# Performance work log

Measured on AMD Instinct MI355X. Metric: run time of the kernel, lower is better.

## Reference

```python
import jax, jax.numpy as jnp
import numpy as np

BIG_NUMBER = 1000000.0
B, N, H = 8, 256, 128   # batch, nodes, node/hidden feat
E, G = 128, 128         # edge feat, graph feat
MID, OUT = 128, 128
IN_Z = 2 * H


def setup_inputs() -> dict:
    key = jax.random.key(0)
    ks = jax.random.split(key, 20)
    sc = lambda fan_in: 1.0 / np.sqrt(fan_in)
    inp = {
        "node_fts": jax.random.normal(ks[0], (B, N, H), jnp.float32),
        "edge_fts": jax.random.normal(ks[1], (B, N, N, E), jnp.float32),
        "graph_fts": jax.random.normal(ks[2], (B, G), jnp.float32),
        "adj_mat": (jax.random.uniform(ks[3], (B, N, N)) < 0.5).astype(jnp.float32),
        "hidden": jax.random.normal(ks[4], (B, N, H), jnp.float32),
        # linear params, stored [in, out]
        "W1": jax.random.normal(ks[5], (IN_Z, MID), jnp.float32) * sc(IN_Z),
        "b1": jnp.zeros((MID,), jnp.float32),
        "W2": jax.random.normal(ks[6], (IN_Z, MID), jnp.float32) * sc(IN_Z),
        "b2": jnp.zeros((MID,), jnp.float32),
        "We": jax.random.normal(ks[7], (E, MID), jnp.float32) * sc(E),
        "be": jnp.zeros((MID,), jnp.float32),
        "Wg": jax.random.normal(ks[8], (G, MID), jnp.float32) * sc(G),
        "bg": jnp.zeros((MID,), jnp.float32),
        "Wo1": jax.random.normal(ks[9], (IN_Z, OUT), jnp.float32) * sc(IN_Z),
        "bo1": jnp.zeros((OUT,), jnp.float32),
        "Wo2": jax.random.normal(ks[10], (MID, OUT), jnp.float32) * sc(MID),
        "bo2": jnp.zeros((OUT,), jnp.float32),
    }
    return inp


def reference(node_fts, edge_fts, graph_fts, adj_mat, hidden,
              W1, b1, W2, b2, We, be, Wg, bg, Wo1, bo1, Wo2, bo2):
    # z: [b, n, 2h]
    z = jnp.concatenate([node_fts, hidden], axis=-1)
    msg_1 = z @ W1 + b1                       # [b, n, mid]
    msg_2 = z @ W2 + b2                       # [b, n, mid]
    msg_e = edge_fts @ We + be                # [b, n, n, mid]
    msg_g = graph_fts @ Wg + bg               # [b, mid]
    # msgs[b, i, j, :]; reduce over i (senders)
    msgs = (msg_1[:, None, :, :] + msg_2[:, :, None, :]
            + msg_e + msg_g[:, None, None, :])
    maxarg = jnp.where(adj_mat[..., None] > 0, msgs, -BIG_NUMBER)
    msgs_red = jnp.max(maxarg, axis=1)        # [b, n, mid]
    ret = jax.nn.relu((z @ Wo1 + bo1) + (msgs_red @ Wo2 + bo2))
    return ret
```

## Files before the change

kernel.cpp:

```cpp
#include <hip/hip_runtime.h>
#include <hip/hip_bf16.h>
#include <stdint.h>
#include <stddef.h>

#define B_   8
#define N_   256
#define H_   128
#define E_   128
#define INZ  256
#define BIGN 1000000.0f

typedef float f32x4 __attribute__((ext_vector_type(4)));
typedef short bf16x8 __attribute__((ext_vector_type(8)));

static __device__ __forceinline__ unsigned cvt2(float a, float b) {
    unsigned short ra = __builtin_bit_cast(unsigned short, __float2bfloat16(a));
    unsigned short rb = __builtin_bit_cast(unsigned short, __float2bfloat16(b));
    return (unsigned)ra | ((unsigned)rb << 16);
}

__global__ __launch_bounds__(256) void prep_kernel(
    const float* __restrict__ node, const float* __restrict__ hidden,
    const float* __restrict__ gf,
    const float* __restrict__ W1, const float* __restrict__ b1,
    const float* __restrict__ W2, const float* __restrict__ b2,
    const float* __restrict__ Wg, const float* __restrict__ bg,
    const float* __restrict__ Wo1, const float* __restrict__ bo1,
    const float* __restrict__ We,
    float* __restrict__ msg1, float* __restrict__ m2g,
    float* __restrict__ zo1, unsigned short* __restrict__ weT)
{
    __shared__ float zs[4][INZ];
    const int t  = threadIdx.x;
    const int r0 = blockIdx.x * 4;
    const int b  = r0 >> 8;

    for (int idx = t; idx < 4 * INZ; idx += 256) {
        int r = idx >> 8, k = idx & 255;
        int row = r0 + r;
        zs[r][k] = (k < H_) ? node[(size_t)row * H_ + k]
                            : hidden[(size_t)row * H_ + (k - H_)];
    }
    if (blockIdx.x < 8) {
        int e0 = blockIdx.x * 2048;
        for (int e = e0 + t; e < e0 + 2048; e += 256) {
            int n = e >> 7, k = e & 127;
            weT[(n * 128 + k) ^ ((n & 7) << 3)] =
                (unsigned short)__builtin_bit_cast(unsigned short,
                    __float2bfloat16(We[k * 128 + n]));
        }
    }
    __syncthreads();

    const int col = t & 127;
    const int rg  = t >> 7;
    float a1[2] = {0, 0}, a2[2] = {0, 0}, ao[2] = {0, 0};

#pragma unroll 4
    for (int k = 0; k < INZ; ++k) {
        float w1 = W1[k * 128 + col];
        float w2 = W2[k * 128 + col];
        float wo = Wo1[k * 128 + col];
#pragma unroll
        for (int rr = 0; rr < 2; ++rr) {
            float zv = zs[rg * 2 + rr][k];
            a1[rr] = fmaf(zv, w1, a1[rr]);
            a2[rr] = fmaf(zv, w2, a2[rr]);
            ao[rr] = fmaf(zv, wo, ao[rr]);
        }
    }
    float mg = bg[col];
#pragma unroll 4
    for (int g = 0; g < 128; ++g)
        mg = fmaf(gf[b * 128 + g], Wg[g * 128 + col], mg);

    const float bb1 = b1[col], bb2 = b2[col], bbo = bo1[col];
#pragma unroll
    for (int rr = 0; rr < 2; ++rr) {
        size_t row = (size_t)(r0 + rg * 2 + rr);
        msg1[row * 128 + col] = a1[rr] + bb1;
        m2g[row * 128 + col]  = a2[rr] + bb2 + mg;
        zo1[row * 128 + col]  = ao[rr] + bbo;
    }
}

__global__ __launch_bounds__(256, 3) void pgn_main(
    const float* __restrict__ edge, const float* __restrict__ adj,
    const float* __restrict__ m2g,
    const unsigned short* __restrict__ weT,
    float* __restrict__ redp, int nsplit)
{
    __shared__ __align__(16) short atile[64 * 128];
    __shared__ __align__(16) short wlds[128 * 128];

    const int t    = threadIdx.x;
    const int lane = t & 63, wid = t >> 6;
    const int wr   = wid >> 1, wn = wid & 1;
    const int hi   = lane >> 4, c15 = lane & 15;
    const int blk  = blockIdx.x;
    const int ih   = blk % nsplit;
    const int jblk = blk / nsplit;
    const int b    = jblk >> 6, jt = jblk & 63;
    const int j0   = jt * 4;
    const int irange = N_ / nsplit;
    const int ibase  = ih * irange;
    const int ntiles = irange >> 4;

    {
        const uint4* wsrc = (const uint4*)weT;
        uint4* wd = (uint4*)wlds;
#pragma unroll
        for (int q = 0; q < 8; ++q) wd[t + 256 * q] = wsrc[t + 256 * q];
    }

    const int th    = t >> 7;
    const int jj_s  = (t >> 5) & 3;
    const int f4c   = t & 31;
    const size_t gbase0 = (((size_t)(b * N_) + ibase + th) * N_ + (j0 + jj_s)) * E_
                          + (size_t)f4c * 4;
    const size_t qstep  = (size_t)2 * N_ * E_;
    const int r0c = 4 * th + jj_s;
    char* lbase = (char*)atile + r0c * 256 + ((f4c * 8) ^ (r0c << 4));

    float rmax[4][4];
#pragma unroll
    for (int n = 0; n < 4; ++n)
#pragma unroll
        for (int rg = 0; rg < 4; ++rg) rmax[n][rg] = -BIGN;

    __syncthreads();

    for (int it = 0; it < ntiles; ++it) {
        const float* gsrc = edge + gbase0 + (size_t)it * 16 * N_ * E_;
        float4 f[8];
#pragma unroll
        for (int q = 0; q < 8; ++q)
            f[q] = *(const float4*)(gsrc + q * qstep);
#pragma unroll
        for (int q = 0; q < 8; ++q) {
            uint2 s;
            s.x = cvt2(f[q].x, f[q].y);
            s.y = cvt2(f[q].z, f[q].w);
            *(uint2*)(lbase + q * 2048) = s;
        }
        __syncthreads();

        float am[2][4], mv[2][4];
#pragma unroll
        for (int m = 0; m < 2; ++m) {
            int ig = ibase + it * 16 + wr * 8 + m * 4 + hi;
            f32x4 a4 = *(const f32x4*)(adj + (size_t)(b * N_ + ig) * N_ + j0);
#pragma unroll
            for (int rg = 0; rg < 4; ++rg) am[m][rg] = a4[rg];
            const float* mp = m2g + (size_t)(b * N_ + ig) * 128 + wn * 64 + c15;
#pragma unroll
            for (int n = 0; n < 4; ++n) mv[m][n] = mp[n * 16];
        }

        f32x4 acc[2][4] = {};
#pragma unroll
        for (int ks = 0; ks < 4; ++ks) {
            bf16x8 af[2], bfv[4];
#pragma unroll
            for (int m = 0; m < 2; ++m) {
                int rowA = wr * 32 + m * 16 + c15;
                int a = (rowA * 256 + ks * 64 + hi * 16) ^ ((rowA & 7) << 4);
                af[m] = *(const bf16x8*)((const char*)atile + a);
            }
#pragma unroll
            for (int n = 0; n < 4; ++n) {
                int rowB = wn * 64 + n * 16 + c15;
                int a = (rowB * 256 + ks * 64 + hi * 16) ^ ((rowB & 7) << 4);
                bfv[n] = *(const bf16x8*)((const char*)wlds + a);
            }
#pragma unroll
            for (int m = 0; m < 2; ++m)
#pragma unroll
                for (int n = 0; n < 4; ++n)
                    acc[m][n] = __builtin_amdgcn_mfma_f32_16x16x32_bf16(
                        af[m], bfv[n], acc[m][n], 0, 0, 0);
        }
        __syncthreads();

#pragma unroll
        for (int m = 0; m < 2; ++m) {
#pragma unroll
            for (int n = 0; n < 4; ++n) {
#pragma unroll
                for (int rg = 0; rg < 4; ++rg) {
                    float v = acc[m][n][rg] + mv[m][n];
                    v = (am[m][rg] > 0.0f) ? v : -BIGN;
                    rmax[n][rg] = fmaxf(rmax[n][rg], v);
                }
            }
        }
    }

#pragma unroll
    for (int n = 0; n < 4; ++n)
#pragma unroll
        for (int rg = 0; rg < 4; ++rg) {
            float v = rmax[n][rg];
            v = fmaxf(v, __shfl_xor(v, 16, 64));
            v = fmaxf(v, __shfl_xor(v, 32, 64));
            rmax[n][rg] = v;
        }
    float* redb = (float*)atile;
    if (wr == 0 && lane < 16) {
#pragma unroll
        for (int n = 0; n < 4; ++n)
#pragma unroll
            for (int rg = 0; rg < 4; ++rg)
                redb[rg * 128 + wn * 64 + n * 16 + c15] = rmax[n][rg];
    }
    __syncthreads();
    if (wr == 1 && lane < 16) {
#pragma unroll
        for (int n = 0; n < 4; ++n)
#pragma unroll
            for (int rg = 0; rg < 4; ++rg) {
                int e = rg * 128 + wn * 64 + n * 16 + c15;
                redb[e] = fmaxf(redb[e], rmax[n][rg]);
            }
    }
    __syncthreads();
#pragma unroll
    for (int e = t; e < 512; e += 256)
        redp[(size_t)blk * 512 + e] = redb[e];
}

__global__ __launch_bounds__(256) void finish_kernel(
    const float* __restrict__ redp, const float* __restrict__ msg1,
    const float* __restrict__ zo1, const float* __restrict__ be,
    const float* __restrict__ Wo2, const float* __restrict__ bo2,
    float* __restrict__ out, int nsplit)
{
    __shared__ float rb[8][128];
    const int t  = threadIdx.x;
    const int r0 = blockIdx.x * 8;

    for (int idx = t; idx < 1024; idx += 256) {
        int rr = idx >> 7, k = idx & 127;
        int r = r0 + rr;
        int jblk = r >> 2, jj = r & 3;
        float v = -BIGN - 1.0f;
        for (int p = 0; p < nsplit; ++p)
            v = fmaxf(v, redp[(size_t)(jblk * nsplit + p) * 512 + jj * 128 + k]);
        rb[rr][k] = v + msg1[(size_t)r * 128 + k] + be[k];
    }
    __syncthreads();

    const int col = t & 127;
    const int half = t >> 7;
#pragma unroll
    for (int rx = 0; rx < 4; ++rx) {
        int rr = half * 4 + rx;
        size_t row = (size_t)(r0 + rr);
        float a = 0.0f;
#pragma unroll 8
        for (int k = 0; k < 128; ++k)
            a = fmaf(rb[rr][k], Wo2[k * 128 + col], a);
        float o = zo1[row * 128 + col] + bo2[col] + a;
        out[row * 128 + col] = fmaxf(o, 0.0f);
    }
}

extern "C" void kernel_launch(void* const* d_in, const int* in_sizes, int n_in,
                              void* d_out, int out_size, void* d_ws, size_t ws_size,
                              hipStream_t stream) {
    const float* node   = (const float*)d_in[0];
    const float* edge   = (const float*)d_in[1];
    const float* gf     = (const float*)d_in[2];
    const float* adj    = (const float*)d_in[3];
    const float* hidden = (const float*)d_in[4];
    const float* W1  = (const float*)d_in[5];
    const float* b1  = (const float*)d_in[6];
    const float* W2  = (const float*)d_in[7];
    const float* b2  = (const float*)d_in[8];
    const float* We  = (const float*)d_in[9];
    const float* be  = (const float*)d_in[10];
    const float* Wg  = (const float*)d_in[11];
    const float* bg  = (const float*)d_in[12];
    const float* Wo1 = (const float*)d_in[13];
    const float* bo1 = (const float*)d_in[14];
    const float* Wo2 = (const float*)d_in[15];
    const float* bo2 = (const float*)d_in[16];
    float* out = (float*)d_out;

    float* msg1 = (float*)d_ws;
    float* m2g  = msg1 + 2048 * 128;
    float* zo1  = m2g + 2048 * 128;
    unsigned short* weT = (unsigned short*)(zo1 + 2048 * 128);
    float* redp = (float*)((char*)weT + 128 * 128 * sizeof(unsigned short));

    const size_t base_bytes = 3u * 1048576u + 32768u;
    int nsplit = (ws_size >= base_bytes + 2u * 1048576u) ? 2 : 1;

    hipLaunchKernelGGL(prep_kernel, dim3(512), dim3(256), 0, stream,
                       node, hidden, gf, W1, b1, W2, b2, Wg, bg, Wo1, bo1, We,
                       msg1, m2g, zo1, weT);
    hipLaunchKernelGGL(pgn_main, dim3(512 * nsplit), dim3(256), 0, stream,
                       edge, adj, m2g, weT, redp, nsplit);
    hipLaunchKernelGGL(finish_kernel, dim3(256), dim3(256), 0, stream,
                       redp, msg1, zo1, be, Wo2, bo2, out, nsplit);
}
```

Before: 110.0 us.

## Stream edge tiles via async global-to-LDS loads with triple buffering

The main kernel now uses global_load_lds to copy fp32 edge tiles straight into a triple-buffered shared-memory ring. Each iteration prefetches the next 8-row tile while computing on the current one, with manual vmcnt waits replacing the full syncthreads pairs. The bf16 conversion moves from the store path to the fragment read, and the We^T fragments are held in registers instead of LDS. This is meant to overlap HBM traffic with MFMA work and cut barrier stalls, at the cost of fp32 LDS footprint (48KB), more register pressure, and fragile hand-counted wait values.

Measured after the change: 106.2 us. 3.5% less time.

```diff
diff --git a/kernel.cpp b/kernel.cpp
--- a/kernel.cpp
+++ b/kernel.cpp
@@ -18,6 +18,19 @@
     unsigned short rb = __builtin_bit_cast(unsigned short, __float2bfloat16(b));
     return (unsigned)ra | ((unsigned)rb << 16);
 }
+
+static __device__ __forceinline__ bf16x8 mk_frag(f32x4 lo, f32x4 h4) {
+    union { unsigned u[4]; bf16x8 v; } r;
+    r.u[0] = cvt2(lo.x, lo.y);
+    r.u[1] = cvt2(lo.z, lo.w);
+    r.u[2] = cvt2(h4.x, h4.y);
+    r.u[3] = cvt2(h4.z, h4.w);
+    return r.v;
+}
+
+#define GL16(gp, lp) __builtin_amdgcn_global_load_lds(                        \
+    (const __attribute__((address_space(1))) unsigned int*)(gp),              \
+    (__attribute__((address_space(3))) unsigned int*)(lp), 16, 0, 0)
 
 __global__ __launch_bounds__(256) void prep_kernel(
     const float* __restrict__ node, const float* __restrict__ hidden,
@@ -86,12 +99,10 @@
 
 __global__ __launch_bounds__(256, 3) void pgn_main(
     const float* __restrict__ edge, const float* __restrict__ adj,
-    const float* __restrict__ m2g,
-    const unsigned short* __restrict__ weT,
+    const float* __restrict__ m2g, const unsigned short* __restrict__ weT,
     float* __restrict__ redp, int nsplit)
 {
-    __shared__ __align__(16) short atile[64 * 128];
-    __shared__ __align__(16) short wlds[128 * 128];
+    __shared__ __align__(16) char smem[49152];
 
     const int t    = threadIdx.x;
     const int lane = t & 63, wid = t >> 6;
@@ -104,23 +115,50 @@
     const int j0   = jt * 4;
     const int irange = N_ / nsplit;
     const int ibase  = ih * irange;
-    const int ntiles = irange >> 4;
-
+    const int nt     = irange >> 3;
+
+    bf16x8 bfr[4][4];
+#pragma unroll
+    for (int n = 0; n < 4; ++n) {
+        int col = wn * 64 + n * 16 + c15;
+        int sw  = (col & 7) << 3;
+#pragma unroll
+        for (int ks = 0; ks < 4; ++ks) {
+            int sidx = (col * 128 + ks * 32 + hi * 8) ^ sw;
+            bfr[n][ks] = *(const bf16x8*)(weT + sidx);
+        }
+    }
+
+    const int l2 = lane >> 5;
+    const int wb = (lane & 31) * 16;
+    const char* gq0; const char* gq1; const char* gq2; const char* gq3;
     {
-        const uint4* wsrc = (const uint4*)weT;
-        uint4* wd = (uint4*)wlds;
-#pragma unroll
-        for (int q = 0; q < 8; ++q) wd[t + 256 * q] = wsrc[t + 256 * q];
-    }
-
-    const int th    = t >> 7;
-    const int jj_s  = (t >> 5) & 3;
-    const int f4c   = t & 31;
-    const size_t gbase0 = (((size_t)(b * N_) + ibase + th) * N_ + (j0 + jj_s)) * E_
-                          + (size_t)f4c * 4;
-    const size_t qstep  = (size_t)2 * N_ * E_;
-    const int r0c = 4 * th + jj_s;
-    char* lbase = (char*)atile + r0c * 256 + ((f4c * 8) ^ (r0c << 4));
+        const char* eb = (const char*)edge;
+#pragma unroll
+        for (int q = 0; q < 4; ++q) {
+            int tr = wid * 8 + 2 * q + l2;
+            int il = tr >> 2, jj = tr & 3;
+            int sb = wb ^ ((tr & 7) << 4);
+            const char* g = eb +
+                (((size_t)(b * N_) + ibase + il) * N_ + (j0 + jj)) * 512 + sb;
+            if (q == 0) gq0 = g; else if (q == 1) gq1 = g;
+            else if (q == 2) gq2 = g; else gq3 = g;
+        }
+    }
+    const unsigned woff = (unsigned)__builtin_amdgcn_readfirstlane(wid * 4096);
+
+    char* pa = smem;
+    char* pb = smem + 16384;
+    char* pc = smem + 32768;
+
+    GL16(gq0, pa + woff);
+    GL16(gq1, pa + woff + 1024);
+    GL16(gq2, pa + woff + 2048);
+    GL16(gq3, pa + woff + 3072);
+
+    const int trc = wr * 16 + c15;
+    const unsigned abase = (unsigned)((trc * 512 + hi * 32) ^ ((trc & 7) << 4));
+    const int il_l = wr * 4 + hi;
 
     float rmax[4][4];
 #pragma unroll
@@ -128,72 +166,48 @@
 #pragma unroll
         for (int rg = 0; rg < 4; ++rg) rmax[n][rg] = -BIGN;
 
-    __syncthreads();
-
-    for (int it = 0; it < ntiles; ++it) {
-        const float* gsrc = edge + gbase0 + (size_t)it * 16 * N_ * E_;
-        float4 f[8];
-#pragma unroll
-        for (int q = 0; q < 8; ++q)
-            f[q] = *(const float4*)(gsrc + q * qstep);
-#pragma unroll
-        for (int q = 0; q < 8; ++q) {
-            uint2 s;
-            s.x = cvt2(f[q].x, f[q].y);
-            s.y = cvt2(f[q].z, f[q].w);
-            *(uint2*)(lbase + q * 2048) = s;
-        }
-        __syncthreads();
-
-        float am[2][4], mv[2][4];
-#pragma unroll
-        for (int m = 0; m < 2; ++m) {
-            int ig = ibase + it * 16 + wr * 8 + m * 4 + hi;
-            f32x4 a4 = *(const f32x4*)(adj + (size_t)(b * N_ + ig) * N_ + j0);
-#pragma unroll
-            for (int rg = 0; rg < 4; ++rg) am[m][rg] = a4[rg];
-            const float* mp = m2g + (size_t)(b * N_ + ig) * 128 + wn * 64 + c15;
-#pragma unroll
-            for (int n = 0; n < 4; ++n) mv[m][n] = mp[n * 16];
-        }
-
-        f32x4 acc[2][4] = {};
+    for (int it = 0; it < nt; ++it) {
+        const int ig = ibase + it * 8 + il_l;
+        f32x4 a4 = *(const f32x4*)(adj + (size_t)(b * N_ + ig) * N_ + j0);
+        const float* mp = m2g + (size_t)(b * N_ + ig) * 128 + wn * 64 + c15;
+        float mv0 = mp[0], mv1 = mp[16], mv2 = mp[32], mv3 = mp[48];
+
+        if (it + 1 < nt) {
+            size_t toff = (size_t)(it + 1) * (8u * N_ * E_ * 4u);
+            GL16(gq0 + toff, pb + woff);
+            GL16(gq1 + toff, pb + woff + 1024);
+            GL16(gq2 + toff, pb + woff + 2048);
+            GL16(gq3 + toff, pb + woff + 3072);
+            asm volatile("s_waitcnt vmcnt(9)" ::: "memory");
+        } else {
+            asm volatile("s_waitcnt vmcnt(5)" ::: "memory");
+        }
+        __builtin_amdgcn_s_barrier();
+        __builtin_amdgcn_sched_barrier(0);
+
+        f32x4 acc[4] = {};
 #pragma unroll
         for (int ks = 0; ks < 4; ++ks) {
-            bf16x8 af[2], bfv[4];
-#pragma unroll
-            for (int m = 0; m < 2; ++m) {
-                int rowA = wr * 32 + m * 16 + c15;
-                int a = (rowA * 256 + ks * 64 + hi * 16) ^ ((rowA & 7) << 4);
-                af[m] = *(const bf16x8*)((const char*)atile + a);
+            f32x4 lo = *(const f32x4*)(pa + (abase + ks * 128));
+            f32x4 h4 = *(const f32x4*)(pa + ((abase ^ 16) + ks * 128));
+            bf16x8 af = mk_frag(lo, h4);
+#pragma unroll
+            for (int n = 0; n < 4; ++n)
+                acc[n] = __builtin_amdgcn_mfma_f32_16x16x32_bf16(
+                    af, bfr[n][ks], acc[n], 0, 0, 0);
+        }
+
+        float mvs[4] = {mv0, mv1, mv2, mv3};
+#pragma unroll
+        for (int n = 0; n < 4; ++n)
+#pragma unroll
+            for (int rg = 0; rg < 4; ++rg) {
+                float v = acc[n][rg] + mvs[n];
+                v = (a4[rg] > 0.0f) ? v : -BIGN;
+                rmax[n][rg] = fmaxf(rmax[n][rg], v);
             }
-#pragma unroll
-            for (int n = 0; n < 4; ++n) {
-                int rowB = wn * 64 + n * 16 + c15;
-                int a = (rowB * 256 + ks * 64 + hi * 16) ^ ((rowB & 7) << 4);
-                bfv[n] = *(const bf16x8*)((const char*)wlds + a);
-            }
-#pragma unroll
-            for (int m = 0; m < 2; ++m)
-#pragma unroll
-                for (int n = 0; n < 4; ++n)
-                    acc[m][n] = __builtin_amdgcn_mfma_f32_16x16x32_bf16(
-                        af[m], bfv[n], acc[m][n], 0, 0, 0);
-        }
-        __syncthreads();
-
-#pragma unroll
-        for (int m = 0; m < 2; ++m) {
-#pragma unroll
-            for (int n = 0; n < 4; ++n) {
-#pragma unroll
-                for (int rg = 0; rg < 4; ++rg) {
-                    float v = acc[m][n][rg] + mv[m][n];
-                    v = (am[m][rg] > 0.0f) ? v : -BIGN;
-                    rmax[n][rg] = fmaxf(rmax[n][rg], v);
-                }
-            }
-        }
+
+        char* tp = pa; pa = pb; pb = pc; pc = tp;
     }
 
 #pragma unroll
@@ -205,7 +219,8 @@
             v = fmaxf(v, __shfl_xor(v, 32, 64));
             rmax[n][rg] = v;
         }
-    float* redb = (float*)atile;
+    __syncthreads();
+    float* redb = (float*)smem;
     if (wr == 0 && lane < 16) {
 #pragma unroll
         for (int n = 0; n < 4; ++n)
@@ -224,7 +239,6 @@
             }
     }
     __syncthreads();
-#pragma unroll
     for (int e = t; e < 512; e += 256)
         redp[(size_t)blk * 512 + e] = redb[e];
 }
```
